# Performance work log

Hardware: AMD Instinct MI355X
Metric: run time of the kernel (lower is better)

The kernel has to match this reference:

```python
import jax, jax.numpy as jnp
import numpy as np

T = 4.0  # distillation temperature (init kwarg)
B, C = 64, 1000


def _hierarchical_softmax(x, targets):
    # x, targets: [B, C]
    xd = jax.lax.stop_gradient(x)
    # t2[b,i,k] = relu(x[b,i] - stop_grad(x[b,k]))  -> [B, C, C]
    t2 = jnp.maximum(x[:, :, None] - xd[:, None, :], 0.0)
    # t3[b,i] = mean_k targets[b,k] * t2[b,i,k]
    t3 = (targets[:, None, :] * t2).mean(axis=-1)  # [B, C]
    choice = targets * jnp.exp(-t3) + (1.0 - targets)
    ex = jnp.exp(x)
    neg_sum = ((1.0 - targets) * ex).sum(axis=-1, keepdims=True)  # [B, 1]
    return ex / (choice * neg_sum + ex)


def setup_inputs() -> dict:
    key = jax.random.key(0)
    k1, k2, k3 = jax.random.split(key, 3)
    y_s = jax.random.normal(k1, (B, C), dtype=jnp.float32)
    y_t = jax.random.normal(k2, (B, C), dtype=jnp.float32)
    w = jax.random.randint(k3, (B, C), 0, 2).astype(jnp.float32)  # multi-hot targets
    return {"y_s": y_s, "y_t": y_t, "w": w}


def reference(y_s, y_t, w):
    # 'w' branch of DistillKL.forward (dead code: preds/thr/sigmoid/max_min omitted)
    p_s = _hierarchical_softmax(y_s / 4.0, w)
    p_t = _hierarchical_softmax(y_t / 4.0, w)
    p_s_1 = jnp.minimum(p_s, 1.0)  # clamp(max=1)
    p_t_1 = jnp.minimum(p_t, 1.0)
    # abs(...) >= 0 so clamp(min=0,max=1) == min(.,1)
    pos_expo = w * jnp.minimum(jnp.abs((p_t_1 + 1.0) / 2.0 - p_s_1), 1.0) ** 0.25
    neg_expo = (1.0 - w) * jnp.minimum(jnp.abs(p_t_1 / 2.0 - p_s_1), 1.0)
    expt = pos_expo + neg_expo
    ps = jnp.maximum(p_s_1 ** expt, 1e-7)
    pt = jnp.maximum(p_t, 1e-7)
    # my_kl: -(target * log(pred)).sum(dim=1).mean() * T**2
    return -(pt * jnp.log(ps)).sum(axis=1).mean() * (T * T)
```

## Files before the change

kernel.cpp:

```cpp
#include <hip/hip_runtime.h>


#define BN 64
#define CN 1000
#define CPAD 1024
#define SPLITS 8
#define CHUNK 125
#define THREADS 512
#define NEG_LOG_EPS -16.118095650958319f

__global__ __launch_bounds__(THREADS) void distill_part(
    const float* __restrict__ ys, const float* __restrict__ yt,
    const float* __restrict__ w, float* __restrict__ part)
{
    const int b = blockIdx.x;
    const int s = blockIdx.y;
    const int tid = threadIdx.x;
    const int lane = tid & 63;
    const int wid = tid >> 6;

    __shared__ __align__(16) float xs[CPAD], xt[CPAD];
    __shared__ __align__(16) float xsc[CPAD], xtc[CPAD];
    __shared__ float wsh[CPAD];
    __shared__ __align__(16) float ps0s[THREADS], ps1s[THREADS];
    __shared__ __align__(16) float ps0t[THREADS], ps1t[THREADS];
    __shared__ float redns[16];
    __shared__ float redterm[2];
    __shared__ int mcnt;

    const float* ysr = ys + b * CN;
    const float* ytr = yt + b * CN;
    const float* wr  = w  + b * CN;

    float ns_s = 0.f, ns_t = 0.f;
    #pragma unroll
    for (int k = tid; k < CPAD; k += THREADS) {
        if (k < CN) {
            float a  = ysr[k] * 0.25f;
            float c2 = ytr[k] * 0.25f;
            float wk = wr[k];
            xs[k] = a; xt[k] = c2; wsh[k] = wk;
            float nw = 1.f - wk;
            ns_s += nw * expf(a);
            ns_t += nw * expf(c2);
        } else {
            xs[k] = 0.f; xt[k] = 0.f; wsh[k] = 0.f;
        }
    }
    #pragma unroll
    for (int off = 32; off > 0; off >>= 1) {
        ns_s += __shfl_down(ns_s, off);
        ns_t += __shfl_down(ns_t, off);
    }
    if (lane == 0) { redns[wid * 2] = ns_s; redns[wid * 2 + 1] = ns_t; }
    __syncthreads();
    float negsum_s = 0.f, negsum_t = 0.f;
    #pragma unroll
    for (int u = 0; u < 8; ++u) {
        negsum_s += redns[u * 2];
        negsum_t += redns[u * 2 + 1];
    }

    if (wid == 0) {
        int base = 0;
        for (int k0 = 0; k0 < CPAD; k0 += 64) {
            const int k = k0 + lane;
            const bool pos = (wsh[k] != 0.f);
            const unsigned long long mask = __ballot(pos);
            const int pre = __popcll(mask & ((1ull << lane) - 1ull));
            if (pos) { xsc[base + pre] = xs[k]; xtc[base + pre] = xt[k]; }
            base += __popcll(mask);
        }
        const int mp = (base + 31) & ~31;
        for (int m = base + lane; m < mp; m += 64) { xsc[m] = 1e30f; xtc[m] = 1e30f; }
        if (lane == 0) mcnt = mp;
    }
    __syncthreads();

    const int Mpad = mcnt;
    const int SL4  = Mpad >> 5;
    const int il = tid & 63;
    const int q  = tid >> 6;
    const int i0 = s * CHUNK + il;
    const bool has2 = (il < CHUNK - 64);
    const int i1 = has2 ? i0 + 64 : i0;
    const float xsi0 = xs[i0], xti0 = xt[i0];
    const float xsi1 = xs[i1], xti1 = xt[i1];
    const float4* s4 = reinterpret_cast<const float4*>(xsc) + q * SL4;
    const float4* t4 = reinterpret_cast<const float4*>(xtc) + q * SL4;
    float a0s = 0.f, a1s = 0.f, a0t = 0.f, a1t = 0.f;
    #pragma unroll 2
    for (int j = 0; j < SL4; ++j) {
        const float4 vs = s4[j];
        const float4 vt = t4[j];
        a0s += (fmaxf(xsi0 - vs.x, 0.f) + fmaxf(xsi0 - vs.y, 0.f))
             + (fmaxf(xsi0 - vs.z, 0.f) + fmaxf(xsi0 - vs.w, 0.f));
        a1s += (fmaxf(xsi1 - vs.x, 0.f) + fmaxf(xsi1 - vs.y, 0.f))
             + (fmaxf(xsi1 - vs.z, 0.f) + fmaxf(xsi1 - vs.w, 0.f));
        a0t += (fmaxf(xti0 - vt.x, 0.f) + fmaxf(xti0 - vt.y, 0.f))
             + (fmaxf(xti0 - vt.z, 0.f) + fmaxf(xti0 - vt.w, 0.f));
        a1t += (fmaxf(xti1 - vt.x, 0.f) + fmaxf(xti1 - vt.y, 0.f))
             + (fmaxf(xti1 - vt.z, 0.f) + fmaxf(xti1 - vt.w, 0.f));
    }
    ps0s[tid] = a0s; ps1s[tid] = a1s;
    ps0t[tid] = a0t; ps1t[tid] = a1t;
    __syncthreads();

    float term = 0.f;
    if (tid < CHUNK) {
        const int i = s * CHUNK + tid;
        const float* bs = (tid < 64) ? ps0s : ps1s;
        const float* bt = (tid < 64) ? ps0t : ps1t;
        const int off = tid & 63;
        float acc_s = 0.f, acc_t = 0.f;
        #pragma unroll
        for (int qq = 0; qq < 8; ++qq) {
            acc_s += bs[qq * 64 + off];
            acc_t += bt[qq * 64 + off];
        }
        const float t3s = acc_s * (1.0f / CN);
        const float t3t = acc_t * (1.0f / CN);
        const float wi = wsh[i];
        const float xsi = xs[i], xti = xt[i];
        const float ch_s = wi * expf(-t3s) + (1.f - wi);
        const float ch_t = wi * expf(-t3t) + (1.f - wi);
        const float exs = expf(xsi), ext = expf(xti);
        const float p_s = exs / (ch_s * negsum_s + exs);
        const float p_t = ext / (ch_t * negsum_t + ext);
        const float ps1 = fminf(p_s, 1.f);
        const float pt1 = fminf(p_t, 1.f);
        const float vpos = fminf(fabsf((pt1 + 1.f) * 0.5f - ps1), 1.f);
        const float vneg = fminf(fabsf(pt1 * 0.5f - ps1), 1.f);
        const float expt = wi * sqrtf(sqrtf(vpos)) + (1.f - wi) * vneg;
        const float logps = fmaxf(expt * logf(ps1), NEG_LOG_EPS);
        term = fmaxf(p_t, 1e-7f) * logps;
    }
    #pragma unroll
    for (int off = 32; off > 0; off >>= 1) term += __shfl_down(term, off);
    if (wid < 2 && lane == 0) redterm[wid] = term;
    __syncthreads();
    if (tid == 0) part[b * SPLITS + s] = redterm[0] + redterm[1];
}

__global__ __launch_bounds__(64) void distill_final(
    const float* __restrict__ part, float* __restrict__ out)
{
    const int t = threadIdx.x;
    float v = 0.f;
    for (int j = t; j < BN * SPLITS; j += 64) v += part[j];
    #pragma unroll
    for (int off = 32; off > 0; off >>= 1) v += __shfl_down(v, off);
    if (t == 0) out[0] = -0.25f * v;
}

extern "C" void kernel_launch(void* const* d_in, const int* in_sizes, int n_in,
                              void* d_out, int out_size, void* d_ws, size_t ws_size,
                              hipStream_t stream) {
    const float* ys = (const float*)d_in[0];
    const float* yt = (const float*)d_in[1];
    const float* w  = (const float*)d_in[2];
    float* out  = (float*)d_out;
    float* part = (float*)d_ws;

    dim3 grid(BN, SPLITS);
    distill_part<<<grid, THREADS, 0, stream>>>(ys, yt, w, part);
    distill_final<<<1, 64, 0, stream>>>(part, out);
}
```

Baseline: 68.45 us.

## Fuse final reduction via atomics and parallelize positive-index compaction across warps

```diff
diff --git a/kernel.cpp b/kernel.cpp
--- a/kernel.cpp
+++ b/kernel.cpp
@@ -7,11 +7,13 @@
 #define SPLITS 8
 #define CHUNK 125
 #define THREADS 512
+#define NBLOCKS (BN * SPLITS)
 #define NEG_LOG_EPS -16.118095650958319f
 
-__global__ __launch_bounds__(THREADS) void distill_part(
+__global__ __launch_bounds__(THREADS, 4) void distill_fused(
     const float* __restrict__ ys, const float* __restrict__ yt,
-    const float* __restrict__ w, float* __restrict__ part)
+    const float* __restrict__ w, float* __restrict__ hdr,
+    float* __restrict__ out)
 {
     const int b = blockIdx.x;
     const int s = blockIdx.y;
@@ -26,7 +28,7 @@
     __shared__ __align__(16) float ps0t[THREADS], ps1t[THREADS];
     __shared__ float redns[16];
     __shared__ float redterm[2];
-    __shared__ int mcnt;
+    __shared__ int segcnt[8];
 
     const float* ysr = ys + b * CN;
     const float* ytr = yt + b * CN;
@@ -61,24 +63,36 @@
         negsum_t += redns[u * 2 + 1];
     }
 
-    if (wid == 0) {
-        int base = 0;
-        for (int k0 = 0; k0 < CPAD; k0 += 64) {
-            const int k = k0 + lane;
-            const bool pos = (wsh[k] != 0.f);
-            const unsigned long long mask = __ballot(pos);
-            const int pre = __popcll(mask & ((1ull << lane) - 1ull));
-            if (pos) { xsc[base + pre] = xs[k]; xtc[base + pre] = xt[k]; }
-            base += __popcll(mask);
-        }
-        const int mp = (base + 31) & ~31;
-        for (int m = base + lane; m < mp; m += 64) { xsc[m] = 1e30f; xtc[m] = 1e30f; }
-        if (lane == 0) mcnt = mp;
+    const int kA = wid * 128 + lane;
+    const int kB = kA + 64;
+    const bool posA = (wsh[kA] != 0.f);
+    const bool posB = (wsh[kB] != 0.f);
+    const unsigned long long mA = __ballot(posA);
+    const unsigned long long mB = __ballot(posB);
+    const int cA = __popcll(mA);
+    if (lane == 0) segcnt[wid] = cA + __popcll(mB);
+    __syncthreads();
+    int base = 0, tot = 0;
+    #pragma unroll
+    for (int u = 0; u < 8; ++u) {
+        const int cu = segcnt[u];
+        if (u < wid) base += cu;
+        tot += cu;
     }
+    const unsigned long long ltmask = (1ull << lane) - 1ull;
+    if (posA) {
+        const int d = base + __popcll(mA & ltmask);
+        xsc[d] = xs[kA]; xtc[d] = xt[kA];
+    }
+    if (posB) {
+        const int d = base + cA + __popcll(mB & ltmask);
+        xsc[d] = xs[kB]; xtc[d] = xt[kB];
+    }
+    const int Mpad = (tot + 31) & ~31;
+    for (int m = tot + tid; m < Mpad; m += THREADS) { xsc[m] = 1e30f; xtc[m] = 1e30f; }
     __syncthreads();
 
-    const int Mpad = mcnt;
-    const int SL4  = Mpad >> 5;
+    const int SL4 = Mpad >> 5;
     const int il = tid & 63;
     const int q  = tid >> 6;
     const int i0 = s * CHUNK + il;
@@ -139,18 +153,17 @@
     for (int off = 32; off > 0; off >>= 1) term += __shfl_down(term, off);
     if (wid < 2 && lane == 0) redterm[wid] = term;
     __syncthreads();
-    if (tid == 0) part[b * SPLITS + s] = redterm[0] + redterm[1];
-}
 
-__global__ __launch_bounds__(64) void distill_final(
-    const float* __restrict__ part, float* __restrict__ out)
-{
-    const int t = threadIdx.x;
-    float v = 0.f;
-    for (int j = t; j < BN * SPLITS; j += 64) v += part[j];
-    #pragma unroll
-    for (int off = 32; off > 0; off >>= 1) v += __shfl_down(v, off);
-    if (t == 0) out[0] = -0.25f * v;
+    if (tid == 0) {
+        const float bsum = redterm[0] + redterm[1];
+        atomicAdd(&hdr[0], bsum);
+        __threadfence();
+        const unsigned old = atomicAdd(reinterpret_cast<unsigned*>(&hdr[1]), 1u);
+        if (old == NBLOCKS - 1) {
+            const float total = atomicAdd(&hdr[0], 0.0f);
+            out[0] = -0.25f * total;
+        }
+    }
 }
 
 extern "C" void kernel_launch(void* const* d_in, const int* in_sizes, int n_in,
@@ -159,10 +172,10 @@
     const float* ys = (const float*)d_in[0];
     const float* yt = (const float*)d_in[1];
     const float* w  = (const float*)d_in[2];
-    float* out  = (float*)d_out;
-    float* part = (float*)d_ws;
+    float* out = (float*)d_out;
+    float* hdr = (float*)d_ws;
 
+    hipMemsetAsync(hdr, 0, 8, stream);
     dim3 grid(BN, SPLITS);
-    distill_part<<<grid, THREADS, 0, stream>>>(ys, yt, w, part);
-    distill_final<<<1, 64, 0, stream>>>(part, out);
+    distill_fused<<<grid, THREADS, 0, stream>>>(ys, yt, w, hdr, out);
 }
```

Result: slower. 76.99 us (+12.5%).
